# Optimization experiments

Hardware: AMD Instinct MI355X
Metric: run time of the kernel (lower is better)

The kernel has to match this reference:

```python
import jax, jax.numpy as jnp
import numpy as np

E = 2048        # embed_dim
H = 16          # num_heads
HKV = 4         # num_heads_kv (GQA)
D = 128         # head_dim
DCONV = 4       # causal depthwise conv width
ROT_DIM = 128   # rotary_emb_dim (= head_dim, full rotation)
ROT_BASE = 10000.0
QKV_DIM = D * (H + 2 * HKV)  # 3072
B, S = 2, 2048


def setup_inputs() -> dict:
    key = jax.random.key(0)
    ks = jax.random.split(key, 7)
    return {
        "x": jax.random.normal(ks[0], (B, S, E), jnp.float32),
        "W_in": jax.random.normal(ks[1], (E, QKV_DIM), jnp.float32) * 0.02,
        "b_in": jax.random.normal(ks[2], (QKV_DIM,), jnp.float32) * 0.02,
        "conv_w": jax.random.normal(ks[3], (QKV_DIM, DCONV), jnp.float32) * 0.1,
        "conv_b": jax.random.normal(ks[4], (QKV_DIM,), jnp.float32) * 0.02,
        "W_out": jax.random.normal(ks[5], (E, E), jnp.float32) * 0.02,
        "b_out": jax.random.normal(ks[6], (E,), jnp.float32) * 0.02,
    }


def _rotary_cos_sin(seqlen, dtype):
    # flash_attn RotaryEmbedding: inv_freq over even indices
    inv_freq = 1.0 / (ROT_BASE ** (np.arange(0, ROT_DIM, 2, dtype=np.float32) / ROT_DIM))
    t = np.arange(seqlen, dtype=np.float32)
    freqs = np.outer(t, inv_freq)                      # [S, ROT_DIM/2]
    return jnp.asarray(np.cos(freqs), dtype), jnp.asarray(np.sin(freqs), dtype)


def _apply_rotary(xh, cos, sin):
    # non-interleaved: rotate halves of the first ROT_DIM dims. xh: [B,S,h,D]
    x1 = xh[..., : ROT_DIM // 2]
    x2 = xh[..., ROT_DIM // 2 : ROT_DIM]
    c = cos[None, :, None, :]
    s = sin[None, :, None, :]
    rot = jnp.concatenate([x1 * c - x2 * s, x2 * c + x1 * s], axis=-1)
    return jnp.concatenate([rot, xh[..., ROT_DIM:]], axis=-1)


def _forward(x, W_in, b_in, conv_w, conv_b, W_out, b_out):
    b, s, _ = x.shape
    qkv = x @ W_in + b_in                              # [B,S,QKV_DIM]

    # causal depthwise conv1d (kernel DCONV, left-pad DCONV-1, trim right)
    xp = jnp.pad(qkv, ((0, 0), (DCONV - 1, 0), (0, 0)))
    conv = conv_b
    for k in range(DCONV):
        conv = conv + xp[:, k : k + s, :] * conv_w[:, k]
    qkv = conv                                         # [B,S,QKV_DIM]

    q, kv = jnp.split(qkv, [H * D], axis=-1)
    q = q.reshape(b, s, H, D)
    kv = kv.reshape(b, s, 2, HKV, D)
    k, v = kv[:, :, 0], kv[:, :, 1]                    # [B,S,HKV,D]

    cos, sin = _rotary_cos_sin(s, x.dtype)
    q = _apply_rotary(q, cos, sin)
    k = _apply_rotary(k, cos, sin)

    # GQA: repeat kv heads
    rep = H // HKV
    k = jnp.repeat(k, rep, axis=2)                     # [B,S,H,D]
    v = jnp.repeat(v, rep, axis=2)

    scale = 1.0 / np.sqrt(D)
    scores = jnp.einsum("bqhd,bkhd->bhqk", q, k) * scale
    causal = jnp.tril(jnp.ones((s, s), bool))
    scores = jnp.where(causal[None, None], scores, jnp.finfo(scores.dtype).min)
    probs = jax.nn.softmax(scores, axis=-1)
    ctx = jnp.einsum("bhqk,bkhd->bqhd", probs, v)      # [B,S,H,D]

    return ctx.reshape(b, s, H * D) @ W_out + b_out    # [B,S,E]


def reference(x, W_in, b_in, conv_w, conv_b, W_out, b_out):
    return _forward(x, W_in, b_in, conv_w, conv_b, W_out, b_out)
```

## Files before the change

kernel.cpp:

```cpp
#include <hip/hip_runtime.h>
#include <hip/hip_bf16.h>

#define B_    2
#define S_    2048
#define E_    2048
#define H_    16
#define HKV_  4
#define D_    128
#define QKV_  3072

#define LOG2E  1.4426950408889634f
#define SCALE  0.08838834764831845f
#define SL     0.127517431f
#define DEFER_THR 8.0f

typedef __attribute__((ext_vector_type(8))) short short8;
typedef __attribute__((ext_vector_type(4))) float floatx4;

typedef __attribute__((address_space(1))) const unsigned int gu32;
typedef __attribute__((address_space(3))) unsigned int lu32;

__device__ __forceinline__ void load_lds16(const unsigned short* g, unsigned short* l) {
    __builtin_amdgcn_global_load_lds((gu32*)g, (lu32*)l, 16, 0, 0);
}

__device__ __forceinline__ float b2f(unsigned short u) {
    union { unsigned int i; float f; } v; v.i = ((unsigned int)u) << 16; return v.f;
}
__device__ __forceinline__ unsigned short f2b(float f) {
    union { float f; unsigned int i; } v; v.f = f;
    unsigned int r = v.i + 0x7FFFu + ((v.i >> 16) & 1u);
    return (unsigned short)(r >> 16);
}
__device__ __forceinline__ unsigned int fbits(float f) {
    union { float f; unsigned int i; } v; v.f = f; return v.i;
}
__device__ __forceinline__ float bits2f(unsigned int i) {
    union { unsigned int i; float f; } v; v.i = i; return v.f;
}

template<int N> __device__ __forceinline__ void waitcnt_vm() {
    static_assert(N >= 0 && N <= 8, "vmcnt out of range");
    if constexpr (N == 0) asm volatile("s_waitcnt vmcnt(0)" ::: "memory");
    else if constexpr (N == 1) asm volatile("s_waitcnt vmcnt(1)" ::: "memory");
    else if constexpr (N == 2) asm volatile("s_waitcnt vmcnt(2)" ::: "memory");
    else if constexpr (N == 3) asm volatile("s_waitcnt vmcnt(3)" ::: "memory");
    else if constexpr (N == 4) asm volatile("s_waitcnt vmcnt(4)" ::: "memory");
    else if constexpr (N == 5) asm volatile("s_waitcnt vmcnt(5)" ::: "memory");
    else if constexpr (N == 6) asm volatile("s_waitcnt vmcnt(6)" ::: "memory");
    else if constexpr (N == 7) asm volatile("s_waitcnt vmcnt(7)" ::: "memory");
    else asm volatile("s_waitcnt vmcnt(8)" ::: "memory");
}

__global__ __launch_bounds__(256) void cvt_f32_bf16(
    const float* __restrict__ src, unsigned short* __restrict__ dst, int n)
{
    int i = (blockIdx.x * 256 + threadIdx.x) * 4;
    if (i + 3 < n) {
        float4 v = *(const float4*)&src[i];
        ushort4 o;
        o.x = f2b(v.x); o.y = f2b(v.y); o.z = f2b(v.z); o.w = f2b(v.w);
        *(ushort4*)&dst[i] = o;
    }
}

__global__ __launch_bounds__(256) void transpose_f32_bf16(
    const float* __restrict__ src, unsigned short* __restrict__ dst,
    int R, int C)
{
    __shared__ unsigned short tile[32][33];
    const int c0 = blockIdx.x * 32, r0 = blockIdx.y * 32;
    const int tx = threadIdx.x, ty = threadIdx.y;
    #pragma unroll
    for (int i = 0; i < 4; i++)
        tile[ty + 8 * i][tx] = f2b(src[(size_t)(r0 + ty + 8 * i) * C + c0 + tx]);
    __syncthreads();
    #pragma unroll
    for (int i = 0; i < 4; i++)
        dst[(size_t)(c0 + ty + 8 * i) * R + r0 + tx] = tile[tx][ty + 8 * i];
}

__global__ __launch_bounds__(256) void transpose_bf16(
    const unsigned short* __restrict__ src, unsigned short* __restrict__ dst,
    int R, int C)
{
    __shared__ unsigned short tile[32][33];
    const size_t boff = (size_t)blockIdx.z * R * C;
    src += boff; dst += boff;
    const int c0 = blockIdx.x * 32, r0 = blockIdx.y * 32;
    const int tx = threadIdx.x, ty = threadIdx.y;
    #pragma unroll
    for (int i = 0; i < 4; i++)
        tile[ty + 8 * i][tx] = src[(size_t)(r0 + ty + 8 * i) * C + c0 + tx];
    __syncthreads();
    #pragma unroll
    for (int i = 0; i < 4; i++)
        dst[(size_t)(c0 + ty + 8 * i) * R + r0 + tx] = tile[tx][ty + 8 * i];
}

template<int WR, int QR, int LX>
__device__ __forceinline__ void stage_unit8(
    const unsigned short* __restrict__ G, unsigned short* ls,
    int uu, int g0, int K, int k0, int wave, int lane)
{
    #pragma unroll
    for (int l = 0; l < LX; ++l) {
        const int c    = wave * LX + l;
        const int rr   = c / (QR / 8);
        const int row0 = rr * WR + uu * QR + (c % (QR / 8)) * 8;
        const int srow = row0 + (lane >> 3);
        const int sg   = (lane & 7) ^ (lane >> 3);
        load_lds16(&G[(size_t)(g0 + srow) * K + k0 + sg * 8], &ls[row0 * 64]);
    }
}

__device__ __forceinline__ void stage_b64(
    const unsigned short* __restrict__ G, unsigned short* ls,
    int u, int g0, int K, int k0, int wave, int lane)
{
    const int row0 = u * 64 + wave * 8;
    const int srow = row0 + (lane >> 3);
    const int sg   = (lane & 7) ^ (lane >> 3);
    load_lds16(&G[(size_t)(g0 + srow) * K + k0 + sg * 8], &ls[row0 * 64]);
}

#define G192_KTILE(ASP, BSP, SA, SB, K1, DO_STAGE)                                 \
  {                                                                                \
    const unsigned short* Asp_ = (ASP);                                            \
    const unsigned short* Bsp_ = (BSP);                                            \
    unsigned short* SA_ = (SA);                                                    \
    unsigned short* SB_ = (SB);                                                    \
    const int k1_ = (K1);                                                          \
    _Pragma("unroll")                                                              \
    for (int p = 0; p < 4; ++p) {                                                  \
      const int qm = p >> 1, qn = p & 1;                                           \
      short8 af[2][2], bg[2][3];                                                   \
      _Pragma("unroll")                                                            \
      for (int ks = 0; ks < 2; ++ks) {                                             \
        _Pragma("unroll")                                                          \
        for (int i = 0; i < 2; ++i)                                                \
          af[ks][i] = *(const short8*)&Asp_[(wm * 64 + qm * 32 + i * 16 + ln) * 64 \
                                            + (((ks * 4 + kq) ^ (ln & 7)) * 8)];  \
        _Pragma("unroll")                                                          \
        for (int j = 0; j < 3; ++j)                                               \
          bg[ks][j] = *(const short8*)&Bsp_[(wn * 96 + qn * 48 + j * 16 + ln) * 64 \
                                            + (((ks * 4 + kq) ^ (ln & 7)) * 8)];  \
      }                                                                            \
      if (DO_STAGE) {                                                              \
        if (p < 3) stage_b64(Bt, SB_, p, n0, K, k1_, wave, lane);                  \
        else {                                                                     \
          stage_unit8<64, 32, 2>(A, SA_, 0, m0, K, k1_, wave, lane);               \
          stage_unit8<64, 32, 2>(A, SA_, 1, m0, K, k1_, wave, lane);               \
        }                                                                          \
      }                                                                            \
      __builtin_amdgcn_s_barrier();                                                \
      __builtin_amdgcn_s_setprio(1);                                               \
      _Pragma("unroll")                                                            \
      for (int ks = 0; ks < 2; ++ks)                                               \
        _Pragma("unroll")                                                          \
        for (int i = 0; i < 2; ++i)                                                \
          _Pragma("unroll")                                                        \
          for (int j = 0; j < 3; ++j)                                              \
            acc[qm * 2 + i][qn * 3 + j] = __builtin_amdgcn_mfma_f32_16x16x32_bf16( \
                af[ks][i], bg[ks][j], acc[qm * 2 + i][qn * 3 + j], 0, 0, 0);       \
      __builtin_amdgcn_s_setprio(0);                                               \
      if (DO_STAGE) {                                                              \
        if (p == 1)      waitcnt_vm<2>();                                          \
        else if (p == 3) waitcnt_vm<2>();                                          \
      }                                                                            \
      __builtin_amdgcn_s_barrier();                                                \
    }                                                                              \
  }

__global__ __launch_bounds__(512, 2) void gemm1_192(
    const unsigned short* __restrict__ A, const unsigned short* __restrict__ Bt,
    const float* __restrict__ bias, unsigned short* __restrict__ C,
    int M, int N, int K)
{
    constexpr int BM = 256, BN = 192;
    constexpr int TILE = (BM + BN) * 64;

    __shared__ unsigned short lds[2 * TILE];

    const int tid  = threadIdx.x;
    const int wave = tid >> 6, lane = tid & 63;
    const int ln   = lane & 15, kq = lane >> 4;
    const int wm   = wave >> 1, wn = wave & 1;

    const int nwg = gridDim.x;
    const int wg  = (blockIdx.x & 7) * (nwg >> 3) + (blockIdx.x >> 3);
    const int nbn = N / BN;
    const int m0  = (wg / nbn) * BM, n0 = (wg % nbn) * BN;

    floatx4 acc[4][6];
    #pragma unroll
    for (int i = 0; i < 4; ++i)
        #pragma unroll
        for (int j = 0; j < 6; ++j) {
            acc[i][j][0] = 0.f; acc[i][j][1] = 0.f;
            acc[i][j][2] = 0.f; acc[i][j][3] = 0.f;
        }

    stage_b64(Bt, &lds[BM * 64], 0, n0, K, 0, wave, lane);
    stage_b64(Bt, &lds[BM * 64], 1, n0, K, 0, wave, lane);
    stage_b64(Bt, &lds[BM * 64], 2, n0, K, 0, wave, lane);
    stage_unit8<64, 32, 2>(A, &lds[0], 0, m0, K, 0, wave, lane);
    stage_unit8<64, 32, 2>(A, &lds[0], 1, m0, K, 0, wave, lane);
    waitcnt_vm<2>();
    __builtin_amdgcn_s_barrier();

    const int NT = K >> 6;

    for (int t = 0; t < NT - 2; t += 2) {
        G192_KTILE(&lds[0],    &lds[BM * 64],        &lds[TILE], &lds[TILE + BM * 64], (t + 1) << 6, true);
        G192_KTILE(&lds[TILE], &lds[TILE + BM * 64], &lds[0],    &lds[BM * 64],        (t + 2) << 6, true);
    }
    G192_KTILE(&lds[0], &lds[BM * 64], &lds[TILE], &lds[TILE + BM * 64], (NT - 1) << 6, true);
    asm volatile("s_waitcnt vmcnt(0)" ::: "memory");
    __builtin_amdgcn_s_barrier();
    G192_KTILE(&lds[TILE], &lds[TILE + BM * 64], &lds[0], &lds[BM * 64], 0, false);

    #pragma unroll
    for (int nj = 0; nj < 6; ++nj) {
        const int col = n0 + wn * 96 + nj * 16 + ln;
        const float bv = bias[col];
        #pragma unroll
        for (int mi = 0; mi < 4; ++mi) {
            const int rowb = m0 + wm * 64 + mi * 16 + kq * 4;
            #pragma unroll
            for (int r = 0; r < 4; ++r)
                C[(size_t)(rowb + r) * N + col] = f2b(acc[mi][nj][r] + bv);
        }
    }
}

#define GEMM8_KTILE(ASP, BSP, SSP, K1, DO_STAGE)                                   \
  {                                                                                \
    const unsigned short* Asp_ = (ASP);                                            \
    const unsigned short* Bsp_ = (BSP);                                            \
    unsigned short* Ssp_ = (SSP);                                                  \
    const int k1_ = (K1);                                                          \
    _Pragma("unroll")                                                              \
    for (int p = 0; p < 4; ++p) {                                                  \
      const int qm = p >> 1, qn = p & 1;                                           \
      short8 af[2][FM], bg[2][FN];                                                 \
      _Pragma("unroll")                                                            \
      for (int ks = 0; ks < 2; ++ks) {                                             \
        _Pragma("unroll")                                                          \
        for (int i = 0; i < FM; ++i)                                               \
          af[ks][i] = *(const short8*)&Asp_[(wm * WMR + qm * QMR + i * 16 + ln) * 64 \
                                            + (((ks * 4 + kq) ^ (ln & 7)) * 8)];  \
        _Pragma("unroll")                                                          \
        for (int j = 0; j < FN; ++j)                                               \
          bg[ks][j] = *(const short8*)&Bsp_[(wn * WNR + qn * QNR + j * 16 + ln) * 64 \
                                            + (((ks * 4 + kq) ^ (ln & 7)) * 8)];  \
      }                                                                            \
      if (DO_STAGE) {                                                              \
        if (p == 0)      stage_unit8<WMR, QMR, LA>(A,  Ssp_,           0, m0, K, k1_, wave, lane); \
        else if (p == 1) stage_unit8<WNR, QNR, LB>(Bt, Ssp_ + BM * 64, 0, n0, K, k1_, wave, lane); \
        else if (p == 2) stage_unit8<WNR, QNR, LB>(Bt, Ssp_ + BM * 64, 1, n0, K, k1_, wave, lane); \
        else             stage_unit8<WMR, QMR, LA>(A,  Ssp_,           1, m0, K, k1_, wave, lane); \
      }                                                                            \
      __builtin_amdgcn_s_barrier();                                                \
      __builtin_amdgcn_s_setprio(1);                                               \
      _Pragma("unroll")                                                            \
      for (int ks = 0; ks < 2; ++ks)                                               \
        _Pragma("unroll")                                                          \
        for (int i = 0; i < FM; ++i)                                               \
          _Pragma("unroll")                                                        \
          for (int j = 0; j < FN; ++j)                                             \
            acc[qm * FM + i][qn * FN + j] = __builtin_amdgcn_mfma_f32_16x16x32_bf16( \
                af[ks][i], bg[ks][j], acc[qm * FM + i][qn * FN + j], 0, 0, 0);     \
      __builtin_amdgcn_s_setprio(0);                                               \
      if (p == 0)      waitcnt_vm<2 * LA>();                                       \
      else if (p == 1) waitcnt_vm<LA + LB>();                                      \
      else if (p == 3) waitcnt_vm<LA + LB>();                                      \
      __builtin_amdgcn_s_barrier();                                                \
    }                                                                              \
  }

template<int BN, int WM, int WN, int OUTF32>
__global__ __launch_bounds__(512, 2) void gemm8(
    const unsigned short* __restrict__ A, const unsigned short* __restrict__ Bt,
    const float* __restrict__ bias, void* __restrict__ Cv,
    int M, int N, int K)
{
    constexpr int BM   = 256;
    constexpr int WMR  = BM / WM, WNR = BN / WN;
    constexpr int QMR  = WMR / 2, QNR = WNR / 2;
    constexpr int FM   = QMR / 16, FN = QNR / 16;
    constexpr int LA   = BM / 128, LB = BN / 128;
    constexpr int TILE = (BM + BN) * 64;

    __shared__ unsigned short lds[2 * TILE];

    const int tid  = threadIdx.x;
    const int wave = tid >> 6, lane = tid & 63;
    const int ln   = lane & 15, kq = lane >> 4;
    const int wm   = wave / WN, wn = wave % WN;

    const int nwg = gridDim.x;
    const int wg  = (blockIdx.x & 7) * (nwg >> 3) + (blockIdx.x >> 3);
    const int nbn = N / BN;
    const int m0  = (wg / nbn) * BM, n0 = (wg % nbn) * BN;

    floatx4 acc[2 * FM][2 * FN];
    #pragma unroll
    for (int i = 0; i < 2 * FM; ++i)
        #pragma unroll
        for (int j = 0; j < 2 * FN; ++j) {
            acc[i][j][0] = 0.f; acc[i][j][1] = 0.f;
            acc[i][j][2] = 0.f; acc[i][j][3] = 0.f;
        }

    stage_unit8<WMR, QMR, LA>(A,  &lds[0],       0, m0, K, 0, wave, lane);
    stage_unit8<WNR, QNR, LB>(Bt, &lds[BM * 64], 0, n0, K, 0, wave, lane);
    stage_unit8<WNR, QNR, LB>(Bt, &lds[BM * 64], 1, n0, K, 0, wave, lane);
    stage_unit8<WMR, QMR, LA>(A,  &lds[0],       1, m0, K, 0, wave, lane);
    waitcnt_vm<LA + LB>();
    __builtin_amdgcn_s_barrier();

    const int NT = K >> 6;

    for (int t = 0; t < NT - 2; t += 2) {
        GEMM8_KTILE(&lds[0],    &lds[BM * 64],        &lds[TILE], (t + 1) << 6, true);
        GEMM8_KTILE(&lds[TILE], &lds[TILE + BM * 64], &lds[0],    (t + 2) << 6, true);
    }
    GEMM8_KTILE(&lds[0], &lds[BM * 64], &lds[TILE], (NT - 1) << 6, true);
    asm volatile("s_waitcnt vmcnt(0)" ::: "memory");
    __builtin_amdgcn_s_barrier();
    GEMM8_KTILE(&lds[TILE], &lds[TILE + BM * 64], &lds[0], 0, false);

    #pragma unroll
    for (int nj = 0; nj < 2 * FN; ++nj) {
        const int col = n0 + wn * WNR + nj * 16 + ln;
        const float bv = bias[col];
        #pragma unroll
        for (int mi = 0; mi < 2 * FM; ++mi) {
            const int rowb = m0 + wm * WMR + mi * 16 + kq * 4;
            #pragma unroll
            for (int r = 0; r < 4; ++r) {
                const float val = acc[mi][nj][r] + bv;
                if (OUTF32) ((float*)Cv)[(size_t)(rowb + r) * N + col] = val;
                else ((unsigned short*)Cv)[(size_t)(rowb + r) * N + col] = f2b(val);
            }
        }
    }
}

__device__ __forceinline__ float conv_at(
    const unsigned short* __restrict__ qb, const float* __restrict__ cw,
    const float* __restrict__ cb, int s, int c)
{
    float acc = cb[c];
    const float* w = cw + c * 4;
    #pragma unroll
    for (int t = 0; t < 4; t++) {
        int sp = s - 3 + t;
        if (sp >= 0) acc += b2f(qb[(size_t)sp * QKV_ + c]) * w[t];
    }
    return acc;
}

__global__ __launch_bounds__(256) void conv_rot(
    const unsigned short* __restrict__ qkv, const float* __restrict__ cw,
    const float* __restrict__ cb, unsigned short* __restrict__ qo,
    unsigned short* __restrict__ ko, unsigned short* __restrict__ vo)
{
    const int bs = blockIdx.x;
    const int b = bs >> 11, s = bs & 2047;
    const unsigned short* qb = qkv + (size_t)b * S_ * QKV_;

    for (int it = threadIdx.x; it < 1792; it += 256) {
        if (it < 1280) {
            const int isq = it < 1024;
            const int rel = isq ? it : it - 1024;
            const int head = rel >> 6, d = rel & 63;
            const int c1 = (isq ? head * 128 : 2048 + head * 128) + d;
            float x1 = conv_at(qb, cw, cb, s, c1);
            float x2 = conv_at(qb, cw, cb, s, c1 + 64);
            float inv = exp2f((float)d * -0.2076205059304601f);
            float ang = (float)s * inv;
            float sn, cs;
            __sincosf(ang, &sn, &cs);
            const float sc = isq ? SL : 1.0f;
            float r1 = (x1 * cs - x2 * sn) * sc;
            float r2 = (x2 * cs + x1 * sn) * sc;
            unsigned short* dst = isq
                ? qo + ((size_t)(b * H_   + head) * S_ + s) * D_
                : ko + ((size_t)(b * HKV_ + head) * S_ + s) * D_;
            dst[d]      = f2b(r1);
            dst[d + 64] = f2b(r2);
        } else {
            const int idx = it - 1280;
            const int g = idx >> 7, d = idx & 127;
            float vv = conv_at(qb, cw, cb, s, 2560 + idx);
            vo[((size_t)(b * HKV_ + g) * S_ + s) * D_ + d] = f2b(vv);
        }
    }
}

__global__ __launch_bounds__(512, 4) void attn(
    const unsigned short* __restrict__ q, const unsigned short* __restrict__ k,
    const unsigned short* __restrict__ vT, unsigned short* __restrict__ ctx)
{
    __shared__ unsigned short Ks[2][64 * 128];
    __shared__ unsigned short Vs[2][128 * 64];
    __shared__ unsigned short Ps[8][16][64];

    const int h = blockIdx.x, qy = blockIdx.y, b = blockIdx.z, g = h >> 2;
    const int qt = b ? (15 - qy) : qy;
    const int tid = threadIdx.x, wave = tid >> 6, lane = tid & 63;
    const int ln = lane & 15, kq = lane >> 4;

    const unsigned short* qh = q  + (size_t)(b * H_   + h) * S_ * D_;
    const unsigned short* kh = k  + (size_t)(b * HKV_ + g) * S_ * D_;
    const unsigned short* vh = vT + (size_t)(b * HKV_ + g) * D_ * S_;

    const int rK = (lane >> 4);
    const int pK = lane & 15;
    const int rV = (lane >> 3);
    const int pV = lane & 7;

    const int qrow0 = qt * 128 + wave * 16;

    short8 qf[4];
    #pragma unroll
    for (int f = 0; f < 4; f++)
        qf[f] = *(const short8*)&qh[(size_t)(qrow0 + ln) * D_ + f * 32 + kq * 8];

    floatx4 o[8];
    #pragma unroll
    for (int i = 0; i < 8; i++) { o[i][0] = 0.f; o[i][1] = 0.f; o[i][2] = 0.f; o[i][3] = 0.f; }
    float mr = -INFINITY, lr = 0.f;

    const int KT = 2 * qt + 2;

    {
        #pragma unroll
        for (int c = 0; c < 2; c++) {
            const int chunk = wave * 2 + c;
            int r  = chunk * 4 + rK;
            int gc = pK ^ (r & 15);
            load_lds16(&kh[(size_t)r * D_ + gc * 8], &Ks[0][chunk * 512]);
            int rv = chunk * 8 + rV;
            int gv = pV ^ (rv & 7);
            load_lds16(&vh[(size_t)rv * S_ + gv * 8], &Vs[0][chunk * 512]);
        }
    }

    for (int kt = 0; kt < KT; kt++) {
        const int buf = kt & 1;
        if (kt + 1 < KT) {
            #pragma unroll
            for (int c = 0; c < 2; c++) {
                const int chunk = wave * 2 + c;
                int r  = chunk * 4 + rK;
                int gc = pK ^ (r & 15);
                load_lds16(&kh[(size_t)((kt + 1) * 64 + r) * D_ + gc * 8],
                           &Ks[buf ^ 1][chunk * 512]);
                int rv = chunk * 8 + rV;
                int gv = pV ^ (rv & 7);
                load_lds16(&vh[(size_t)rv * S_ + (kt + 1) * 64 + gv * 8],
                           &Vs[buf ^ 1][chunk * 512]);
            }
            waitcnt_vm<4>();
        } else {
            waitcnt_vm<0>();
        }
        __builtin_amdgcn_s_barrier();

        if (kt * 64 <= qrow0 + 15) {
            floatx4 scv[4];
            #pragma unroll
            for (int nb = 0; nb < 4; nb++) { scv[nb][0]=0.f; scv[nb][1]=0.f; scv[nb][2]=0.f; scv[nb][3]=0.f; }
            __builtin_amdgcn_s_setprio(1);
            #pragma unroll
            for (int ks = 0; ks < 4; ks++) {
                #pragma unroll
                for (int nb = 0; nb < 4; nb++) {
                    short8 kf = *(const short8*)&Ks[buf][(nb * 16 + ln) * 128 + (((ks * 4 + kq) ^ ln) * 8)];
                    scv[nb] = __builtin_amdgcn_mfma_f32_16x16x32_bf16(kf, qf[ks], scv[nb], 0, 0, 0);
                }
            }
            __builtin_amdgcn_s_setprio(0);

            if (kt * 64 + 63 > qrow0) {
                const int qi = qrow0 + ln;
                #pragma unroll
                for (int nb = 0; nb < 4; nb++)
                    #pragma unroll
                    for (int r = 0; r < 4; r++)
                        if (kt * 64 + nb * 16 + kq * 4 + r > qi) scv[nb][r] = -INFINITY;
            }

            float mx = -INFINITY;
            #pragma unroll
            for (int nb = 0; nb < 4; nb++) {
                float a0 = fmaxf(scv[nb][0], scv[nb][1]);
                float a1 = fmaxf(scv[nb][2], scv[nb][3]);
                mx = fmaxf(mx, fmaxf(a0, a1));
            }
            mx = fmaxf(mx, __shfl_xor(mx, 16));
            mx = fmaxf(mx, __shfl_xor(mx, 32));

            float mt = mr, al = 1.0f;
            if (!__all(mx - mr <= DEFER_THR)) {
                mt = fmaxf(mr, mx);
                al = exp2f(mr - mt);
                mr = mt;
                float alr[4];
                #pragma unroll
                for (int r = 0; r < 4; r++) alr[r] = __shfl(al, kq * 4 + r);
                #pragma unroll
                for (int dn = 0; dn < 8; dn++)
                    #pragma unroll
                    for (int r = 0; r < 4; r++) o[dn][r] *= alr[r];
            }

            float rs = 0.f;
            #pragma unroll
            for (int nb = 0; nb < 4; nb++) {
                const int gct = 2 * nb + (kq >> 1);
                const int pbase = ((gct ^ (ln & 7)) << 3) + ((kq & 1) << 2);
                #pragma unroll
                for (int rr = 0; rr < 2; rr++) {
                    unsigned int u0 = fbits(exp2f(scv[nb][2 * rr]     - mt));
                    unsigned int u1 = fbits(exp2f(scv[nb][2 * rr + 1] - mt));
                    rs += bits2f(u0 & 0xFFFF0000u) + bits2f(u1 & 0xFFFF0000u);
                    *(unsigned int*)&Ps[wave][ln][pbase + 2 * rr] =
                        (u0 >> 16) | (u1 & 0xFFFF0000u);
                }
            }
            rs += __shfl_xor(rs, 16);
            rs += __shfl_xor(rs, 32);
            lr = lr * al + rs;

            short8 pa0 = *(const short8*)&Ps[wave][ln][(kq ^ (ln & 7)) << 3];
            short8 pa1 = *(const short8*)&Ps[wave][ln][((4 + kq) ^ (ln & 7)) << 3];
            __builtin_amdgcn_s_setprio(1);
            #pragma unroll
            for (int dn = 0; dn < 8; dn++) {
                short8 b0 = *(const short8*)&Vs[buf][(dn * 16 + ln) * 64 + ((kq ^ (ln & 7)) * 8)];
                o[dn] = __builtin_amdgcn_mfma_f32_16x16x32_bf16(pa0, b0, o[dn], 0, 0, 0);
                short8 b1 = *(const short8*)&Vs[buf][(dn * 16 + ln) * 64 + (((4 + kq) ^ (ln & 7)) * 8)];
                o[dn] = __builtin_amdgcn_mfma_f32_16x16x32_bf16(pa1, b1, o[dn], 0, 0, 0);
            }
            __builtin_amdgcn_s_setprio(0);
        }

        __builtin_amdgcn_s_barrier();
    }

    float lrr[4];
    #pragma unroll
    for (int r = 0; r < 4; r++) lrr[r] = 1.0f / __shfl(lr, kq * 4 + r);
    #pragma unroll
    for (int r = 0; r < 4; r++) {
        size_t rowoff = (size_t)(b * S_ + qrow0 + kq * 4 + r) * (H_ * D_) + h * D_;
        #pragma unroll
        for (int dn = 0; dn < 8; dn++)
            ctx[rowoff + dn * 16 + ln] = f2b(o[dn][r] * lrr[r]);
    }
}

extern "C" void kernel_launch(void* const* d_in, const int* in_sizes, int n_in,
                              void* d_out, int out_size, void* d_ws, size_t ws_size,
                              hipStream_t stream)
{
    const float* x     = (const float*)d_in[0];
    const float* W_in  = (const float*)d_in[1];
    const float* b_in  = (const float*)d_in[2];
    const float* cw    = (const float*)d_in[3];
    const float* cb    = (const float*)d_in[4];
    const float* W_out = (const float*)d_in[5];
    const float* b_out = (const float*)d_in[6];
    float* out = (float*)d_out;
    char* ws = (char*)d_ws;

    const size_t MB = 1024 * 1024;
    unsigned short* WtIn  = (unsigned short*)(ws);
    unsigned short* WtOut = (unsigned short*)(ws + 12 * MB);
    unsigned short* x16   = (unsigned short*)(ws + 20 * MB);
    unsigned short* qkv   = (unsigned short*)(ws + 36 * MB);
    unsigned short* qa    = (unsigned short*)(ws + 60 * MB);
    unsigned short* ka    = (unsigned short*)(ws + 76 * MB);
    unsigned short* va    = (unsigned short*)(ws + 80 * MB);
    unsigned short* vTa   = (unsigned short*)(ws + 84 * MB);
    unsigned short* ctx   = (unsigned short*)(ws + 20 * MB);

    dim3 tb(32, 8);
    hipLaunchKernelGGL(cvt_f32_bf16, dim3(8192), dim3(256), 0, stream, x, x16, 8388608);
    hipLaunchKernelGGL(transpose_f32_bf16, dim3(96, 64), tb, 0, stream, W_in,  WtIn,  2048, 3072);
    hipLaunchKernelGGL(transpose_f32_bf16, dim3(64, 64), tb, 0, stream, W_out, WtOut, 2048, 2048);
    hipLaunchKernelGGL(gemm1_192, dim3(256), dim3(512), 0, stream,
                       x16, WtIn, b_in, qkv, 4096, 3072, 2048);
    hipLaunchKernelGGL(conv_rot, dim3(4096), dim3(256), 0, stream, qkv, cw, cb, qa, ka, va);
    hipLaunchKernelGGL(transpose_bf16, dim3(4, 64, 8), tb, 0, stream, va, vTa, 2048, 128);
    hipLaunchKernelGGL(attn, dim3(16, 16, 2), dim3(512), 0, stream, qa, ka, vTa, ctx);
    hipLaunchKernelGGL((gemm8<128, 4, 2, 1>), dim3(256), dim3(512), 0, stream,
                       ctx, WtOut, b_out, (void*)out, 4096, 2048, 2048);
}
```

Before: 346.1 us.

## Hoist B fragments per k-tile in GEMMs and compute softmax row sums via MFMA

Both GEMM k-tile macros now load all B fragments once per k-tile and loop over two M halves instead of four quadrants, so B is read from LDS once per half rather than per quadrant. Staging and waitcnt points are regrouped to match, and the explicit drain plus barrier before the last tile is folded into the macro. The output GEMM template is replaced by a fixed 256x128 kernel. In attention, the per-row sum of probabilities is computed by an MFMA against a vector of ones instead of scalar adds and cross-lane shuffles, which costs two extra MFMAs per block but uses the exact bf16 P values.

```diff
diff --git a/kernel.cpp b/kernel.cpp
--- a/kernel.cpp
+++ b/kernel.cpp
@@ -34,9 +34,6 @@
 }
 __device__ __forceinline__ unsigned int fbits(float f) {
     union { float f; unsigned int i; } v; v.f = f; return v.i;
-}
-__device__ __forceinline__ float bits2f(unsigned int i) {
-    union { unsigned int i; float f; } v; v.i = i; return v.f;
 }
 
 template<int N> __device__ __forceinline__ void waitcnt_vm() {
@@ -124,31 +121,36 @@
     load_lds16(&G[(size_t)(g0 + srow) * K + k0 + sg * 8], &ls[row0 * 64]);
 }
 
-#define G192_KTILE(ASP, BSP, SA, SB, K1, DO_STAGE)                                 \
+
+#define G1_KT(ASP, BSP, SA, SB, K1, DO_STAGE)                                      \
   {                                                                                \
     const unsigned short* Asp_ = (ASP);                                            \
     const unsigned short* Bsp_ = (BSP);                                            \
     unsigned short* SA_ = (SA);                                                    \
     unsigned short* SB_ = (SB);                                                    \
     const int k1_ = (K1);                                                          \
+    short8 bg[2][6];                                                               \
     _Pragma("unroll")                                                              \
-    for (int p = 0; p < 4; ++p) {                                                  \
-      const int qm = p >> 1, qn = p & 1;                                           \
-      short8 af[2][2], bg[2][3];                                                   \
+    for (int ks = 0; ks < 2; ++ks)                                                 \
       _Pragma("unroll")                                                            \
-      for (int ks = 0; ks < 2; ++ks) {                                             \
+      for (int jj = 0; jj < 6; ++jj)                                               \
+        bg[ks][jj] = *(const short8*)&Bsp_[(wn * 96 + jj * 16 + ln) * 64           \
+                                           + (((ks * 4 + kq) ^ (ln & 7)) * 8)];    \
+    _Pragma("unroll")                                                              \
+    for (int qm = 0; qm < 2; ++qm) {                                               \
+      short8 af[2][2];                                                             \
+      _Pragma("unroll")                                                            \
+      for (int ks = 0; ks < 2; ++ks)                                               \
         _Pragma("unroll")                                                          \
         for (int i = 0; i < 2; ++i)                                                \
           af[ks][i] = *(const short8*)&Asp_[(wm * 64 + qm * 32 + i * 16 + ln) * 64 \
-                                            + (((ks * 4 + kq) ^ (ln & 7)) * 8)];  \
-        _Pragma("unroll")                                                          \
-        for (int j = 0; j < 3; ++j)                                               \
-          bg[ks][j] = *(const short8*)&Bsp_[(wn * 96 + qn * 48 + j * 16 + ln) * 64 \
-                                            + (((ks * 4 + kq) ^ (ln & 7)) * 8)];  \
-      }                                                                            \
+                                            + (((ks * 4 + kq) ^ (ln & 7)) * 8)];   \
       if (DO_STAGE) {                                                              \
-        if (p < 3) stage_b64(Bt, SB_, p, n0, K, k1_, wave, lane);                  \
-        else {                                                                     \
+        if (qm == 0) {                                                             \
+          stage_b64(Bt, SB_, 0, n0, K, k1_, wave, lane);                           \
+          stage_b64(Bt, SB_, 1, n0, K, k1_, wave, lane);                           \
+          stage_b64(Bt, SB_, 2, n0, K, k1_, wave, lane);                           \
+        } else {                                                                   \
           stage_unit8<64, 32, 2>(A, SA_, 0, m0, K, k1_, wave, lane);               \
           stage_unit8<64, 32, 2>(A, SA_, 1, m0, K, k1_, wave, lane);               \
         }                                                                          \
@@ -160,14 +162,12 @@
         _Pragma("unroll")                                                          \
         for (int i = 0; i < 2; ++i)                                                \
           _Pragma("unroll")                                                        \
-          for (int j = 0; j < 3; ++j)                                              \
-            acc[qm * 2 + i][qn * 3 + j] = __builtin_amdgcn_mfma_f32_16x16x32_bf16( \
-                af[ks][i], bg[ks][j], acc[qm * 2 + i][qn * 3 + j], 0, 0, 0);       \
+          for (int jj = 0; jj < 6; ++jj)                                           \
+            acc[qm * 2 + i][jj] = __builtin_amdgcn_mfma_f32_16x16x32_bf16(         \
+                af[ks][i], bg[ks][jj], acc[qm * 2 + i][jj], 0, 0, 0);              \
       __builtin_amdgcn_s_setprio(0);                                               \
-      if (DO_STAGE) {                                                              \
-        if (p == 1)      waitcnt_vm<2>();                                          \
-        else if (p == 3) waitcnt_vm<2>();                                          \
-      }                                                                            \
+      if (DO_STAGE) { if (qm == 0) waitcnt_vm<3>(); else waitcnt_vm<2>(); }        \
+      else if (qm == 0) waitcnt_vm<0>();                                           \
       __builtin_amdgcn_s_barrier();                                                \
     }                                                                              \
   }
@@ -212,13 +212,11 @@
     const int NT = K >> 6;
 
     for (int t = 0; t < NT - 2; t += 2) {
-        G192_KTILE(&lds[0],    &lds[BM * 64],        &lds[TILE], &lds[TILE + BM * 64], (t + 1) << 6, true);
-        G192_KTILE(&lds[TILE], &lds[TILE + BM * 64], &lds[0],    &lds[BM * 64],        (t + 2) << 6, true);
-    }
-    G192_KTILE(&lds[0], &lds[BM * 64], &lds[TILE], &lds[TILE + BM * 64], (NT - 1) << 6, true);
-    asm volatile("s_waitcnt vmcnt(0)" ::: "memory");
-    __builtin_amdgcn_s_barrier();
-    G192_KTILE(&lds[TILE], &lds[TILE + BM * 64], &lds[0], &lds[BM * 64], 0, false);
+        G1_KT(&lds[0],    &lds[BM * 64],        &lds[TILE], &lds[TILE + BM * 64], (t + 1) << 6, true);
+        G1_KT(&lds[TILE], &lds[TILE + BM * 64], &lds[0],    &lds[BM * 64],        (t + 2) << 6, true);
+    }
+    G1_KT(&lds[0], &lds[BM * 64], &lds[TILE], &lds[TILE + BM * 64], (NT - 1) << 6, true);
+    G1_KT(&lds[TILE], &lds[TILE + BM * 64], &lds[0], &lds[BM * 64], 0, false);
 
     #pragma unroll
     for (int nj = 0; nj < 6; ++nj) {
@@ -234,62 +232,61 @@
     }
 }
 
-#define GEMM8_KTILE(ASP, BSP, SSP, K1, DO_STAGE)                                   \
+#define G2_KT(ASP, BSP, SA, SB, K1, DO_STAGE)                                      \
   {                                                                                \
     const unsigned short* Asp_ = (ASP);                                            \
     const unsigned short* Bsp_ = (BSP);                                            \
-    unsigned short* Ssp_ = (SSP);                                                  \
+    unsigned short* SA_ = (SA);                                                    \
+    unsigned short* SB_ = (SB);                                                    \
     const int k1_ = (K1);                                                          \
+    short8 bg[2][4];                                                               \
     _Pragma("unroll")                                                              \
-    for (int p = 0; p < 4; ++p) {                                                  \
-      const int qm = p >> 1, qn = p & 1;                                           \
-      short8 af[2][FM], bg[2][FN];                                                 \
+    for (int ks = 0; ks < 2; ++ks)                                                 \
       _Pragma("unroll")                                                            \
-      for (int ks = 0; ks < 2; ++ks) {                                             \
+      for (int jj = 0; jj < 4; ++jj)                                               \
+        bg[ks][jj] = *(const short8*)&Bsp_[(wn * 64 + jj * 16 + ln) * 64           \
+                                           + (((ks * 4 + kq) ^ (ln & 7)) * 8)];    \
+    _Pragma("unroll")                                                              \
+    for (int qm = 0; qm < 2; ++qm) {                                               \
+      short8 af[2][2];                                                             \
+      _Pragma("unroll")                                                            \
+      for (int ks = 0; ks < 2; ++ks)                                               \
         _Pragma("unroll")                                                          \
-        for (int i = 0; i < FM; ++i)                                               \
-          af[ks][i] = *(const short8*)&Asp_[(wm * WMR + qm * QMR + i * 16 + ln) * 64 \
-                                            + (((ks * 4 + kq) ^ (ln & 7)) * 8)];  \
-        _Pragma("unroll")                                                          \
-        for (int j = 0; j < FN; ++j)                                               \
-          bg[ks][j] = *(const short8*)&Bsp_[(wn * WNR + qn * QNR + j * 16 + ln) * 64 \
-                                            + (((ks * 4 + kq) ^ (ln & 7)) * 8)];  \
-      }                                                                            \
+        for (int i = 0; i < 2; ++i)                                                \
+          af[ks][i] = *(const short8*)&Asp_[(wm * 64 + qm * 32 + i * 16 + ln) * 64 \
+                                            + (((ks * 4 + kq) ^ (ln & 7)) * 8)];   \
       if (DO_STAGE) {                                                              \
-        if (p == 0)      stage_unit8<WMR, QMR, LA>(A,  Ssp_,           0, m0, K, k1_, wave, lane); \
-        else if (p == 1) stage_unit8<WNR, QNR, LB>(Bt, Ssp_ + BM * 64, 0, n0, K, k1_, wave, lane); \
-        else if (p == 2) stage_unit8<WNR, QNR, LB>(Bt, Ssp_ + BM * 64, 1, n0, K, k1_, wave, lane); \
-        else             stage_unit8<WMR, QMR, LA>(A,  Ssp_,           1, m0, K, k1_, wave, lane); \
+        if (qm == 0) {                                                             \
+          stage_unit8<64, 32, 1>(Bt, SB_, 0, n0, K, k1_, wave, lane);              \
+          stage_unit8<64, 32, 1>(Bt, SB_, 1, n0, K, k1_, wave, lane);              \
+        } else {                                                                   \
+          stage_unit8<64, 32, 2>(A, SA_, 0, m0, K, k1_, wave, lane);               \
+          stage_unit8<64, 32, 2>(A, SA_, 1, m0, K, k1_, wave, lane);               \
+        }                                                                          \
       }                                                                            \
       __builtin_amdgcn_s_barrier();                                                \
       __builtin_amdgcn_s_setprio(1);                                               \
       _Pragma("unroll")                                                            \
       for (int ks = 0; ks < 2; ++ks)                                               \
         _Pragma("unroll")                                                          \
-        for (int i = 0; i < FM; ++i)                                               \
+        for (int i = 0; i < 2; ++i)                                                \
           _Pragma("unroll")                                                        \
-          for (int j = 0; j < FN; ++j)                                             \
-            acc[qm * FM + i][qn * FN + j] = __builtin_amdgcn_mfma_f32_16x16x32_bf16( \
-                af[ks][i], bg[ks][j], acc[qm * FM + i][qn * FN + j], 0, 0, 0);     \
+          for (int jj = 0; jj < 4; ++jj)                                           \
+            acc[qm * 2 + i][jj] = __builtin_amdgcn_mfma_f32_16x16x32_bf16(         \
+                af[ks][i], bg[ks][jj], acc[qm * 2 + i][jj], 0, 0, 0);              \
       __builtin_amdgcn_s_setprio(0);                                               \
-      if (p == 0)      waitcnt_vm<2 * LA>();                                       \
-      else if (p == 1) waitcnt_vm<LA + LB>();                                      \
-      else if (p == 3) waitcnt_vm<LA + LB>();                                      \
+      if (DO_STAGE) waitcnt_vm<2>();                                               \
+      else if (qm == 0) waitcnt_vm<0>();                                           \
       __builtin_amdgcn_s_barrier();                                                \
     }                                                                              \
   }
 
-template<int BN, int WM, int WN, int OUTF32>
-__global__ __launch_bounds__(512, 2) void gemm8(
+__global__ __launch_bounds__(512, 2) void gemm2_128(
     const unsigned short* __restrict__ A, const unsigned short* __restrict__ Bt,
-    const float* __restrict__ bias, void* __restrict__ Cv,
+    const float* __restrict__ bias, float* __restrict__ C,
     int M, int N, int K)
 {
-    constexpr int BM   = 256;
-    constexpr int WMR  = BM / WM, WNR = BN / WN;
-    constexpr int QMR  = WMR / 2, QNR = WNR / 2;
-    constexpr int FM   = QMR / 16, FN = QNR / 16;
-    constexpr int LA   = BM / 128, LB = BN / 128;
+    constexpr int BM = 256, BN = 128;
     constexpr int TILE = (BM + BN) * 64;
 
     __shared__ unsigned short lds[2 * TILE];
@@ -297,53 +294,48 @@
     const int tid  = threadIdx.x;
     const int wave = tid >> 6, lane = tid & 63;
     const int ln   = lane & 15, kq = lane >> 4;
-    const int wm   = wave / WN, wn = wave % WN;
+    const int wm   = wave >> 1, wn = wave & 1;
 
     const int nwg = gridDim.x;
     const int wg  = (blockIdx.x & 7) * (nwg >> 3) + (blockIdx.x >> 3);
     const int nbn = N / BN;
     const int m0  = (wg / nbn) * BM, n0 = (wg % nbn) * BN;
 
-    floatx4 acc[2 * FM][2 * FN];
-    #pragma unroll
-    for (int i = 0; i < 2 * FM; ++i)
+    floatx4 acc[4][4];
+    #pragma unroll
+    for (int i = 0; i < 4; ++i)
         #pragma unroll
-        for (int j = 0; j < 2 * FN; ++j) {
+        for (int j = 0; j < 4; ++j) {
             acc[i][j][0] = 0.f; acc[i][j][1] = 0.f;
             acc[i][j][2] = 0.f; acc[i][j][3] = 0.f;
         }
 
-    stage_unit8<WMR, QMR, LA>(A,  &lds[0],       0, m0, K, 0, wave, lane);
-    stage_unit8<WNR, QNR, LB>(Bt, &lds[BM * 64], 0, n0, K, 0, wave, lane);
-    stage_unit8<WNR, QNR, LB>(Bt, &lds[BM * 64], 1, n0, K, 0, wave, lane);
-    stage_unit8<WMR, QMR, LA>(A,  &lds[0],       1, m0, K, 0, wave, lane);
-    waitcnt_vm<LA + LB>();
+    stage_unit8<64, 32, 1>(Bt, &lds[BM * 64], 0, n0, K, 0, wave, lane);
+    stage_unit8<64, 32, 1>(Bt, &lds[BM * 64], 1, n0, K, 0, wave, lane);
+    stage_unit8<64, 32, 2>(A, &lds[0], 0, m0, K, 0, wave, lane);
+    stage_unit8<64, 32, 2>(A, &lds[0], 1, m0, K, 0, wave, lane);
+    waitcnt_vm<2>();
     __builtin_amdgcn_s_barrier();
 
     const int NT = K >> 6;
 
     for (int t = 0; t < NT - 2; t += 2) {
-        GEMM8_KTILE(&lds[0],    &lds[BM * 64],        &lds[TILE], (t + 1) << 6, true);
-        GEMM8_KTILE(&lds[TILE], &lds[TILE + BM * 64], &lds[0],    (t + 2) << 6, true);
-    }
-    GEMM8_KTILE(&lds[0], &lds[BM * 64], &lds[TILE], (NT - 1) << 6, true);
-    asm volatile("s_waitcnt vmcnt(0)" ::: "memory");
-    __builtin_amdgcn_s_barrier();
-    GEMM8_KTILE(&lds[TILE], &lds[TILE + BM * 64], &lds[0], 0, false);
-
-    #pragma unroll
-    for (int nj = 0; nj < 2 * FN; ++nj) {
-        const int col = n0 + wn * WNR + nj * 16 + ln;
+        G2_KT(&lds[0],    &lds[BM * 64],        &lds[TILE], &lds[TILE + BM * 64], (t + 1) << 6, true);
+        G2_KT(&lds[TILE], &lds[TILE + BM * 64], &lds[0],    &lds[BM * 64],        (t + 2) << 6, true);
+    }
+    G2_KT(&lds[0], &lds[BM * 64], &lds[TILE], &lds[TILE + BM * 64], (NT - 1) << 6, true);
+    G2_KT(&lds[TILE], &lds[TILE + BM * 64], &lds[0], &lds[BM * 64], 0, false);
+
+    #pragma unroll
+    for (int nj = 0; nj < 4; ++nj) {
+        const int col = n0 + wn * 64 + nj * 16 + ln;
         const float bv = bias[col];
         #pragma unroll
-        for (int mi = 0; mi < 2 * FM; ++mi) {
-            const int rowb = m0 + wm * WMR + mi * 16 + kq * 4;
-            #pragma unroll
-            for (int r = 0; r < 4; ++r) {
-                const float val = acc[mi][nj][r] + bv;
-                if (OUTF32) ((float*)Cv)[(size_t)(rowb + r) * N + col] = val;
-                else ((unsigned short*)Cv)[(size_t)(rowb + r) * N + col] = f2b(val);
-            }
+        for (int mi = 0; mi < 4; ++mi) {
+            const int rowb = m0 + wm * 64 + mi * 16 + kq * 4;
+            #pragma unroll
+            for (int r = 0; r < 4; ++r)
+                C[(size_t)(rowb + r) * N + col] = acc[mi][nj][r] + bv;
         }
     }
 }
@@ -429,10 +421,15 @@
     for (int f = 0; f < 4; f++)
         qf[f] = *(const short8*)&qh[(size_t)(qrow0 + ln) * D_ + f * 32 + kq * 8];
 
+    short8 ones;
+    #pragma unroll
+    for (int j = 0; j < 8; j++) ones[j] = (short)0x3F80;
+
     floatx4 o[8];
     #pragma unroll
     for (int i = 0; i < 8; i++) { o[i][0] = 0.f; o[i][1] = 0.f; o[i][2] = 0.f; o[i][3] = 0.f; }
-    float mr = -INFINITY, lr = 0.f;
+    floatx4 lrv; lrv[0] = 0.f; lrv[1] = 0.f; lrv[2] = 0.f; lrv[3] = 0.f;
+    float mr = -INFINITY;
 
     const int KT = 2 * qt + 2;
 
@@ -494,20 +491,21 @@
                         if (kt * 64 + nb * 16 + kq * 4 + r > qi) scv[nb][r] = -INFINITY;
             }
 
-            float mx = -INFINITY;
-            #pragma unroll
-            for (int nb = 0; nb < 4; nb++) {
-                float a0 = fmaxf(scv[nb][0], scv[nb][1]);
-                float a1 = fmaxf(scv[nb][2], scv[nb][3]);
-                mx = fmaxf(mx, fmaxf(a0, a1));
-            }
+            float mx = fmaxf(fmaxf(scv[0][0], scv[0][1]), scv[0][2]);
+            mx = fmaxf(fmaxf(mx, scv[0][3]), scv[1][0]);
+            mx = fmaxf(fmaxf(mx, scv[1][1]), scv[1][2]);
+            mx = fmaxf(fmaxf(mx, scv[1][3]), scv[2][0]);
+            mx = fmaxf(fmaxf(mx, scv[2][1]), scv[2][2]);
+            mx = fmaxf(fmaxf(mx, scv[2][3]), scv[3][0]);
+            mx = fmaxf(fmaxf(mx, scv[3][1]), scv[3][2]);
+            mx = fmaxf(mx, scv[3][3]);
             mx = fmaxf(mx, __shfl_xor(mx, 16));
             mx = fmaxf(mx, __shfl_xor(mx, 32));
 
-            float mt = mr, al = 1.0f;
+            float mt = mr;
             if (!__all(mx - mr <= DEFER_THR)) {
                 mt = fmaxf(mr, mx);
-                al = exp2f(mr - mt);
+                float al = exp2f(mr - mt);
                 mr = mt;
                 float alr[4];
                 #pragma unroll
@@ -516,9 +514,10 @@
                 for (int dn = 0; dn < 8; dn++)
                     #pragma unroll
                     for (int r = 0; r < 4; r++) o[dn][r] *= alr[r];
+                #pragma unroll
+                for (int r = 0; r < 4; r++) lrv[r] *= alr[r];
             }
 
-            float rs = 0.f;
             #pragma unroll
             for (int nb = 0; nb < 4; nb++) {
                 const int gct = 2 * nb + (kq >> 1);
@@ -527,18 +526,17 @@
                 for (int rr = 0; rr < 2; rr++) {
                     unsigned int u0 = fbits(exp2f(scv[nb][2 * rr]     - mt));
                     unsigned int u1 = fbits(exp2f(scv[nb][2 * rr + 1] - mt));
-                    rs += bits2f(u0 & 0xFFFF0000u) + bits2f(u1 & 0xFFFF0000u);
                     *(unsigned int*)&Ps[wave][ln][pbase + 2 * rr] =
                         (u0 >> 16) | (u1 & 0xFFFF0000u);
                 }
             }
-            rs += __shfl_xor(rs, 16);
-            rs += __shfl_xor(rs, 32);
-            lr = lr * al + rs;
 
             short8 pa0 = *(const short8*)&Ps[wave][ln][(kq ^ (ln & 7)) << 3];
             short8 pa1 = *(const short8*)&Ps[wave][ln][((4 + kq) ^ (ln & 7)) << 3];
             __builtin_amdgcn_s_setprio(1);
+            floatx4 oe; oe[0] = 0.f; oe[1] = 0.f; oe[2] = 0.f; oe[3] = 0.f;
+            oe = __builtin_amdgcn_mfma_f32_16x16x32_bf16(pa0, ones, oe, 0, 0, 0);
+            oe = __builtin_amdgcn_mfma_f32_16x16x32_bf16(pa1, ones, oe, 0, 0, 0);
             #pragma unroll
             for (int dn = 0; dn < 8; dn++) {
                 short8 b0 = *(const short8*)&Vs[buf][(dn * 16 + ln) * 64 + ((kq ^ (ln & 7)) * 8)];
@@ -547,20 +545,20 @@
                 o[dn] = __builtin_amdgcn_mfma_f32_16x16x32_bf16(pa1, b1, o[dn], 0, 0, 0);
             }
             __builtin_amdgcn_s_setprio(0);
+            #pragma unroll
+            for (int r = 0; r < 4; r++) lrv[r] += oe[r];
         }
 
         __builtin_amdgcn_s_barrier();
     }
 
-    float lrr[4];
-    #pragma unroll
-    for (int r = 0; r < 4; r++) lrr[r] = 1.0f / __shfl(lr, kq * 4 + r);
     #pragma unroll
     for (int r = 0; r < 4; r++) {
+        const float lrr = 1.0f / lrv[r];
         size_t rowoff = (size_t)(b * S_ + qrow0 + kq * 4 + r) * (H_ * D_) + h * D_;
         #pragma unroll
         for (int dn = 0; dn < 8; dn++)
-            ctx[rowoff + dn * 16 + ln] = f2b(o[dn][r] * lrr[r]);
+            ctx[rowoff + dn * 16 + ln] = f2b(o[dn][r] * lrr);
     }
 }
 
@@ -598,6 +596,6 @@
     hipLaunchKernelGGL(conv_rot, dim3(4096), dim3(256), 0, stream, qkv, cw, cb, qa, ka, va);
     hipLaunchKernelGGL(transpose_bf16, dim3(4, 64, 8), tb, 0, stream, va, vTa, 2048, 128);
     hipLaunchKernelGGL(attn, dim3(16, 16, 2), dim3(512), 0, stream, qa, ka, vTa, ctx);
-    hipLaunchKernelGGL((gemm8<128, 4, 2, 1>), dim3(256), dim3(512), 0, stream,
-                       ctx, WtOut, b_out, (void*)out, 4096, 2048, 2048);
-}
+    hipLaunchKernelGGL(gemm2_128, dim3(256), dim3(512), 0, stream,
+                       ctx, WtOut, b_out, out, 4096, 2048, 2048);
+}
```

After: 332.3 us. 4.0% less time.
